# Kernel tuning notes

Hardware: AMD Instinct MI355X
Metric: run time of the kernel (lower is better)

Reference implementation:

```python
import jax, jax.numpy as jnp
from jax import lax
import numpy as np

B, T = 64, 512
IN, H, L, OUT = 128, 1024, 3, 1


def setup_inputs() -> dict:
    key = jax.random.key(0)
    ks = jax.random.split(key, 10)
    s = 1.0 / np.sqrt(H)  # PyTorch LSTM init: U(-1/sqrt(H), 1/sqrt(H))
    u = lambda k, shape: jax.random.uniform(k, shape, jnp.float32, -s, s)
    return {
        "x": jax.random.normal(ks[0], (B, T, IN), jnp.float32),
        "W_ih0": u(ks[1], (4 * H, IN)),
        "W_ih1": u(ks[2], (4 * H, H)),
        "W_ih2": u(ks[3], (4 * H, H)),
        "W_hh": u(ks[4], (L, 4 * H, H)),
        "b_ih": u(ks[5], (L, 4 * H)),
        "b_hh": u(ks[6], (L, 4 * H)),
        "fc_w": u(ks[7], (OUT, H)),
        "fc_b": u(ks[8], (OUT,)),
    }


def _lstm_layer(x, W_ih, W_hh_l, b_ih_l, b_hh_l):
    """One LSTM layer, batch_first input [B, T, F] -> [B, T, H].
    PyTorch gate order: i, f, g, o."""
    Bq = x.shape[0]
    Hh = W_hh_l.shape[1]
    # Precompute input projection for all timesteps (one big GEMM).
    xp = jnp.einsum("btf,gf->btg", x, W_ih) + b_ih_l + b_hh_l  # [B, T, 4H]
    xp = jnp.swapaxes(xp, 0, 1)  # [T, B, 4H] for scan

    def step(carry, gates_in):
        h, c = carry
        g = gates_in + h @ W_hh_l.T  # [B, 4H]
        i_, f_, g_, o_ = jnp.split(g, 4, axis=-1)
        c = jax.nn.sigmoid(f_) * c + jax.nn.sigmoid(i_) * jnp.tanh(g_)
        h = jax.nn.sigmoid(o_) * jnp.tanh(c)
        return (h, c), h

    h0 = jnp.zeros((Bq, Hh), x.dtype)
    _, hs = lax.scan(step, (h0, h0), xp)  # hs: [T, B, H]
    return jnp.swapaxes(hs, 0, 1)  # [B, T, H]


def reference(x, W_ih0, W_ih1, W_ih2, W_hh, b_ih, b_hh, fc_w, fc_b):
    # 3-layer LSTM (dropout disabled / eval mode for determinism).
    h = x
    for l, Wih in enumerate((W_ih0, W_ih1, W_ih2)):
        h = _lstm_layer(h, Wih, W_hh[l], b_ih[l], b_hh[l])
    # Original applies fc to all timesteps then takes [:, -1, :];
    # slicing first is mathematically identical and avoids a [B,T,OUT] buffer.
    return h[:, -1, :] @ fc_w.T + fc_b  # [B, OUT]
```

## Files before the change

kernel.cpp:

```cpp
#include <hip/hip_runtime.h>


#define TT 512
#define INF 128
#define HH 1024
#define NBLOCKS 192

typedef _Float16 f16x8 __attribute__((ext_vector_type(8)));
typedef float f32x4 __attribute__((ext_vector_type(4)));

#define HBUF_OFF 1024
#define XBUF_OFF (1024 + 786432)

__device__ __forceinline__ float sigmf(float x) { return 1.f / (1.f + __expf(-x)); }
__device__ __forceinline__ float tanhfast(float x) { return 1.f - 2.f / (__expf(2.f * x) + 1.f); }

__global__ void init_kernel(unsigned* ctrl, unsigned* hbuf_u32, float* out, const float* fcb) {
  int tid = blockIdx.x * 256 + threadIdx.x;
  if (tid < 196608) hbuf_u32[tid] = 0u;
  if (blockIdx.x == 0) {
    if (threadIdx.x < 2) ctrl[threadIdx.x] = 0u;
    if (threadIdx.x >= 64 && threadIdx.x < 128) out[threadIdx.x - 64] = fcb[0];
  }
}

__global__ void packx_kernel(const float* __restrict__ x, _Float16* __restrict__ xbuf) {
  int tid = blockIdx.x * 256 + threadIdx.x;
  int t = tid >> 10;
  int rem = tid & 1023;
  int kk = rem >> 8;
  int bt = (rem >> 6) & 3;
  int lane = rem & 63;
  int b = bt * 16 + (lane & 15);
  int k = kk * 32 + (lane >> 4) * 8;
  const float* src = x + ((size_t)b * TT + t) * INF + k;
  f16x8 v;
#pragma unroll
  for (int j = 0; j < 8; ++j) v[j] = (_Float16)src[j];
  ((f16x8*)xbuf)[tid] = v;
}

__device__ __forceinline__ f16x8 load_frag_agent(const unsigned long long* p) {
  union { unsigned long long u[2]; f16x8 v; } r;
  r.u[0] = __hip_atomic_load(p, __ATOMIC_RELAXED, __HIP_MEMORY_SCOPE_AGENT);
  r.u[1] = __hip_atomic_load(p + 1, __ATOMIC_RELAXED, __HIP_MEMORY_SCOPE_AGENT);
  return r.v;
}

__device__ __forceinline__ void loadB(f16x8 bf[4], int layer, int kk, int t, int rp,
                                      const f16x8* __restrict__ xb8,
                                      const unsigned long long* __restrict__ hb_u,
                                      int lane) {
  if (layer == 0 && kk < 4) {
    const f16x8* bsrc = xb8 + (size_t)t * 1024 + (size_t)kk * 256;
#pragma unroll
    for (int bt = 0; bt < 4; ++bt) bf[bt] = bsrc[bt * 64 + lane];
  } else {
    int buf, kidx;
    if (layer == 0) { buf = rp; kidx = kk - 4; }
    else if (layer == 1) {
      if (kk < 32) { buf = rp; kidx = kk; } else { buf = 2 + rp; kidx = kk - 32; }
    } else {
      if (kk < 32) { buf = 2 + rp; kidx = kk; } else { buf = 4 + rp; kidx = kk - 32; }
    }
#pragma unroll
    for (int bt = 0; bt < 4; ++bt)
      bf[bt] = load_frag_agent(hb_u + ((size_t)buf * 8192 + kidx * 256 + bt * 64 + lane) * 2);
  }
}

__global__ void __launch_bounds__(256, 1)
lstm_main(const float* __restrict__ Wih0, const float* __restrict__ Wih1,
          const float* __restrict__ Wih2, const float* __restrict__ Whh,
          const float* __restrict__ bih, const float* __restrict__ bhh,
          const float* __restrict__ fcw, float* __restrict__ out,
          unsigned* __restrict__ ctrl, _Float16* __restrict__ hbuf,
          const _Float16* __restrict__ xbuf) {
  const int blk = blockIdx.x;
  const int layer = blk >> 6;
  const int cu = blk & 63;
  const int tid = threadIdx.x;
  const int wave = tid >> 6;
  const int lane = tid & 63;
  const int m = lane & 15;
  const int q = lane >> 4;
  const int hid0 = cu << 4;

  const int KW = (layer == 0) ? 9 : 16;
  const int kk0 = wave * KW;

  __shared__ float part[4][4][16][66];
  __shared__ float fcacc[64];

  f16x8 fz;
#pragma unroll
  for (int j = 0; j < 8; ++j) fz[j] = (_Float16)0.f;

  f16x8 afrag[4][16];
#pragma unroll
  for (int g = 0; g < 4; ++g) {
#pragma unroll
    for (int kkl = 0; kkl < 16; ++kkl) {
      afrag[g][kkl] = fz;
      if (kkl < KW) {
        int kk = kk0 + kkl;
        int row = g * HH + hid0 + m;
        const float* src;
        if (layer == 0) {
          src = (kk < 4) ? (Wih0 + (size_t)row * INF + kk * 32)
                         : (Whh + (size_t)row * HH + (kk - 4) * 32);
        } else if (layer == 1) {
          src = (kk < 32) ? (Wih1 + (size_t)row * HH + kk * 32)
                          : (Whh + (size_t)(4 * HH) * HH + (size_t)row * HH + (kk - 32) * 32);
        } else {
          src = (kk < 32) ? (Wih2 + (size_t)row * HH + kk * 32)
                          : (Whh + (size_t)(8 * HH) * HH + (size_t)row * HH + (kk - 32) * 32);
        }
        src += q * 8;
        f16x8 v;
#pragma unroll
        for (int j = 0; j < 8; ++j) v[j] = (_Float16)src[j];
        afrag[g][kkl] = v;
      }
    }
  }

  const int bq = tid & 63;
  const int j4 = wave * 4;
  float biasv[4][4];
#pragma unroll
  for (int g = 0; g < 4; ++g)
#pragma unroll
    for (int i = 0; i < 4; ++i) {
      int row = layer * 4 * HH + g * HH + hid0 + j4 + i;
      biasv[g][i] = bih[row] + bhh[row];
    }
  float fcwv[4];
#pragma unroll
  for (int i = 0; i < 4; ++i) fcwv[i] = (layer == 2) ? fcw[hid0 + j4 + i] : 0.f;
  float cst[4] = {0.f, 0.f, 0.f, 0.f};

  const int jg = hid0 + j4;
  const int kkp = jg >> 5;
  const int qp = (jg >> 3) & 3;
  const int slot = (j4 & 7) >> 2;
  const int btp = bq >> 4;
  const int lanep = (bq & 15) + (qp << 4);

  const f16x8* xb8 = (const f16x8*)xbuf;
  const unsigned long long* hb_u = (const unsigned long long*)hbuf;
  unsigned long long* hb_w = (unsigned long long*)hbuf;

  const f32x4 zacc = {0.f, 0.f, 0.f, 0.f};

  for (int s = 0; s < TT + 2; ++s) {
    const int t = s - layer;
    const bool active = (t >= 0) && (t < TT);
    if (active) {
      const int rp = (s + 1) & 1;
      const int wp = s & 1;

      f32x4 acc[4][4];
#pragma unroll
      for (int g = 0; g < 4; ++g)
#pragma unroll
        for (int bt = 0; bt < 4; ++bt) acc[g][bt] = zacc;

      f16x8 bf0[4], bf1[4], bf2[4], bf3[4];
      loadB(bf0, layer, kk0 + 0, t, rp, xb8, hb_u, lane);
      loadB(bf1, layer, kk0 + 1, t, rp, xb8, hb_u, lane);
      loadB(bf2, layer, kk0 + 2, t, rp, xb8, hb_u, lane);
      loadB(bf3, layer, kk0 + 3, t, rp, xb8, hb_u, lane);

#define LSTM_STEP(KKL, BUF)                                                   \
      if ((KKL) < KW) {                                                       \
        _Pragma("unroll")                                                     \
        for (int g = 0; g < 4; ++g) {                                         \
          _Pragma("unroll")                                                   \
          for (int bt = 0; bt < 4; ++bt)                                      \
            acc[g][bt] = __builtin_amdgcn_mfma_f32_16x16x32_f16(              \
                afrag[g][(KKL)], BUF[bt], acc[g][bt], 0, 0, 0);               \
        }                                                                     \
        if ((KKL) + 4 < KW)                                                   \
          loadB(BUF, layer, kk0 + (KKL) + 4, t, rp, xb8, hb_u, lane);         \
      }

      LSTM_STEP(0, bf0)
      LSTM_STEP(1, bf1)
      LSTM_STEP(2, bf2)
      LSTM_STEP(3, bf3)
      LSTM_STEP(4, bf0)
      LSTM_STEP(5, bf1)
      LSTM_STEP(6, bf2)
      LSTM_STEP(7, bf3)
      LSTM_STEP(8, bf0)
      LSTM_STEP(9, bf1)
      LSTM_STEP(10, bf2)
      LSTM_STEP(11, bf3)
      LSTM_STEP(12, bf0)
      LSTM_STEP(13, bf1)
      LSTM_STEP(14, bf2)
      LSTM_STEP(15, bf3)
#undef LSTM_STEP

#pragma unroll
      for (int g = 0; g < 4; ++g)
#pragma unroll
        for (int bt = 0; bt < 4; ++bt)
#pragma unroll
          for (int r = 0; r < 4; ++r)
            part[wave][g][q * 4 + r][bt * 16 + m] = acc[g][bt][r];

      const bool do_fc = (layer == 2) && (t == TT - 1);
      if (do_fc && tid < 64) fcacc[tid] = 0.f;
      __syncthreads();

      float pre[4][4];
#pragma unroll
      for (int g = 0; g < 4; ++g)
#pragma unroll
        for (int i = 0; i < 4; ++i) pre[g][i] = biasv[g][i];
#pragma unroll
      for (int w = 0; w < 4; ++w)
#pragma unroll
        for (int g = 0; g < 4; ++g)
#pragma unroll
          for (int i = 0; i < 4; ++i) pre[g][i] += part[w][g][j4 + i][bq];

      union { unsigned long long u; _Float16 h4[4]; } pk;
      float facc = 0.f;
#pragma unroll
      for (int i = 0; i < 4; ++i) {
        float ig = sigmf(pre[0][i]);
        float fg = sigmf(pre[1][i]);
        float gg = tanhfast(pre[2][i]);
        float og = sigmf(pre[3][i]);
        cst[i] = fg * cst[i] + ig * gg;
        float hv = og * tanhfast(cst[i]);
        pk.h4[i] = (_Float16)hv;
        facc += hv * fcwv[i];
      }
      unsigned long long* pub =
          hb_w + ((size_t)(((layer * 2 + wp) * 32 + kkp) * 256 + btp * 64 + lanep)) * 2 + slot;
      __hip_atomic_store(pub, pk.u, __ATOMIC_RELAXED, __HIP_MEMORY_SCOPE_AGENT);

      if (do_fc) {
        atomicAdd(&fcacc[bq], facc);
        __syncthreads();
        if (tid < 64) atomicAdd(&out[tid], fcacc[tid]);
      }
    }

    __builtin_amdgcn_s_waitcnt(0);
    __syncthreads();
    if (tid == 0) {
      const unsigned target = (unsigned)(s + 1) * NBLOCKS;
      __hip_atomic_fetch_add(&ctrl[0], 1u, __ATOMIC_RELAXED, __HIP_MEMORY_SCOPE_AGENT);
      while (__hip_atomic_load(&ctrl[0], __ATOMIC_RELAXED, __HIP_MEMORY_SCOPE_AGENT) < target) {
        __builtin_amdgcn_s_sleep(2);
      }
    }
    __syncthreads();
  }
}

extern "C" void kernel_launch(void* const* d_in, const int* in_sizes, int n_in,
                              void* d_out, int out_size, void* d_ws, size_t ws_size,
                              hipStream_t stream) {
  const float* x    = (const float*)d_in[0];
  const float* Wih0 = (const float*)d_in[1];
  const float* Wih1 = (const float*)d_in[2];
  const float* Wih2 = (const float*)d_in[3];
  const float* Whh  = (const float*)d_in[4];
  const float* bih  = (const float*)d_in[5];
  const float* bhh  = (const float*)d_in[6];
  const float* fcw  = (const float*)d_in[7];
  const float* fcb  = (const float*)d_in[8];
  float* out = (float*)d_out;

  char* ws = (char*)d_ws;
  unsigned* ctrl = (unsigned*)ws;
  _Float16* hbuf = (_Float16*)(ws + HBUF_OFF);
  _Float16* xbuf = (_Float16*)(ws + XBUF_OFF);

  init_kernel<<<768, 256, 0, stream>>>(ctrl, (unsigned*)hbuf, out, fcb);
  packx_kernel<<<2048, 256, 0, stream>>>(x, xbuf);
  lstm_main<<<NBLOCKS, 256, 0, stream>>>(Wih0, Wih1, Wih2, Whh, bih, bhh, fcw,
                                         out, ctrl, hbuf, xbuf);
}
```

Baseline: 6.566 ms.

## Hand-pipeline B-fragment loads with inline asm dwordx4 and explicit vmcnt waits

Replaces the per-kk branching loadB (with paired 64-bit agent-scope atomic loads) with specialized per-layer k-loops that issue single 128-bit global loads using cache-bypass bits (sc0 sc1) for the h buffers and cached loads for x. Explicit s_waitcnt vmcnt counts and sched_barriers enforce a 4-deep software pipeline so the MFMAs for one k-slice overlap with loads for later slices. The aim is fewer memory instructions, no runtime layer/kk branching inside the loop, and tighter latency hiding. The risk is in coherence: the new loads are not atomics and rely on the sc bits to see other blocks' writes, and the hard-coded wait counts must stay correct.

```diff
diff --git a/kernel.cpp b/kernel.cpp
--- a/kernel.cpp
+++ b/kernel.cpp
@@ -40,33 +40,88 @@
   ((f16x8*)xbuf)[tid] = v;
 }
 
-__device__ __forceinline__ f16x8 load_frag_agent(const unsigned long long* p) {
-  union { unsigned long long u[2]; f16x8 v; } r;
-  r.u[0] = __hip_atomic_load(p, __ATOMIC_RELAXED, __HIP_MEMORY_SCOPE_AGENT);
-  r.u[1] = __hip_atomic_load(p + 1, __ATOMIC_RELAXED, __HIP_MEMORY_SCOPE_AGENT);
-  return r.v;
-}
-
-__device__ __forceinline__ void loadB(f16x8 bf[4], int layer, int kk, int t, int rp,
-                                      const f16x8* __restrict__ xb8,
-                                      const unsigned long long* __restrict__ hb_u,
-                                      int lane) {
-  if (layer == 0 && kk < 4) {
-    const f16x8* bsrc = xb8 + (size_t)t * 1024 + (size_t)kk * 256;
-#pragma unroll
-    for (int bt = 0; bt < 4; ++bt) bf[bt] = bsrc[bt * 64 + lane];
+__device__ __forceinline__ f16x8 load_ic16(const void* p) {
+  f16x8 v;
+  asm volatile("global_load_dwordx4 %0, %1, off sc0 sc1" : "=&v"(v) : "v"(p) : "memory");
+  return v;
+}
+__device__ __forceinline__ f16x8 load_ca16(const void* p) {
+  f16x8 v;
+  asm volatile("global_load_dwordx4 %0, %1, off" : "=&v"(v) : "v"(p) : "memory");
+  return v;
+}
+
+__device__ __forceinline__ void loadB4_ic(f16x8 bf[4], const char* base, int lane) {
+#pragma unroll
+  for (int bt = 0; bt < 4; ++bt) bf[bt] = load_ic16(base + (size_t)(bt * 64 + lane) * 16);
+}
+
+__device__ __forceinline__ void pfL0(f16x8 bf[4], int kk, const char* xb, const char* bLo,
+                                     int lane) {
+  if (kk < 4) {
+    const char* b = xb + (size_t)kk * 4096;
+#pragma unroll
+    for (int bt = 0; bt < 4; ++bt) bf[bt] = load_ca16(b + (size_t)(bt * 64 + lane) * 16);
   } else {
-    int buf, kidx;
-    if (layer == 0) { buf = rp; kidx = kk - 4; }
-    else if (layer == 1) {
-      if (kk < 32) { buf = rp; kidx = kk; } else { buf = 2 + rp; kidx = kk - 32; }
-    } else {
-      if (kk < 32) { buf = 2 + rp; kidx = kk; } else { buf = 4 + rp; kidx = kk - 32; }
-    }
-#pragma unroll
-    for (int bt = 0; bt < 4; ++bt)
-      bf[bt] = load_frag_agent(hb_u + ((size_t)buf * 8192 + kidx * 256 + bt * 64 + lane) * 2);
-  }
+    const char* b = bLo + (size_t)(kk - 4) * 4096;
+#pragma unroll
+    for (int bt = 0; bt < 4; ++bt) bf[bt] = load_ic16(b + (size_t)(bt * 64 + lane) * 16);
+  }
+}
+
+#define WAITV(N) asm volatile("s_waitcnt vmcnt(" #N ")" ::: "memory")
+#define SB0 __builtin_amdgcn_sched_barrier(0)
+#define MSTEP(KKL, BUF)                                                     \
+  {                                                                         \
+    _Pragma("unroll") for (int g = 0; g < 4; ++g) {                         \
+      _Pragma("unroll") for (int bt = 0; bt < 4; ++bt)                      \
+          acc[g][bt] = __builtin_amdgcn_mfma_f32_16x16x32_f16(              \
+              afrag[g][KKL], BUF[bt], acc[g][bt], 0, 0, 0);                 \
+    }                                                                       \
+  }
+
+__device__ __forceinline__ void kloop16(f32x4 acc[4][4], const f16x8 afrag[4][16], int kk0,
+                                        const char* bLo, const char* bHi, int lane) {
+  const char* wb = (kk0 < 32) ? bLo + (size_t)kk0 * 4096 : bHi + (size_t)(kk0 - 32) * 4096;
+  f16x8 b0[4], b1[4], b2[4], b3[4];
+  loadB4_ic(b0, wb + 0 * 4096, lane);
+  loadB4_ic(b1, wb + 1 * 4096, lane);
+  loadB4_ic(b2, wb + 2 * 4096, lane);
+  loadB4_ic(b3, wb + 3 * 4096, lane);
+  WAITV(12); SB0; MSTEP(0, b0);  loadB4_ic(b0, wb + 4 * 4096, lane);
+  WAITV(12); SB0; MSTEP(1, b1);  loadB4_ic(b1, wb + 5 * 4096, lane);
+  WAITV(12); SB0; MSTEP(2, b2);  loadB4_ic(b2, wb + 6 * 4096, lane);
+  WAITV(12); SB0; MSTEP(3, b3);  loadB4_ic(b3, wb + 7 * 4096, lane);
+  WAITV(12); SB0; MSTEP(4, b0);  loadB4_ic(b0, wb + 8 * 4096, lane);
+  WAITV(12); SB0; MSTEP(5, b1);  loadB4_ic(b1, wb + 9 * 4096, lane);
+  WAITV(12); SB0; MSTEP(6, b2);  loadB4_ic(b2, wb + 10 * 4096, lane);
+  WAITV(12); SB0; MSTEP(7, b3);  loadB4_ic(b3, wb + 11 * 4096, lane);
+  WAITV(12); SB0; MSTEP(8, b0);  loadB4_ic(b0, wb + 12 * 4096, lane);
+  WAITV(12); SB0; MSTEP(9, b1);  loadB4_ic(b1, wb + 13 * 4096, lane);
+  WAITV(12); SB0; MSTEP(10, b2); loadB4_ic(b2, wb + 14 * 4096, lane);
+  WAITV(12); SB0; MSTEP(11, b3); loadB4_ic(b3, wb + 15 * 4096, lane);
+  WAITV(12); SB0; MSTEP(12, b0);
+  WAITV(8);  SB0; MSTEP(13, b1);
+  WAITV(4);  SB0; MSTEP(14, b2);
+  WAITV(0);  SB0; MSTEP(15, b3);
+}
+
+__device__ __forceinline__ void kloop9(f32x4 acc[4][4], const f16x8 afrag[4][16], int kk0,
+                                       const char* xb, const char* bLo, int lane) {
+  f16x8 b0[4], b1[4], b2[4], b3[4];
+  pfL0(b0, kk0 + 0, xb, bLo, lane);
+  pfL0(b1, kk0 + 1, xb, bLo, lane);
+  pfL0(b2, kk0 + 2, xb, bLo, lane);
+  pfL0(b3, kk0 + 3, xb, bLo, lane);
+  WAITV(12); SB0; MSTEP(0, b0); pfL0(b0, kk0 + 4, xb, bLo, lane);
+  WAITV(12); SB0; MSTEP(1, b1); pfL0(b1, kk0 + 5, xb, bLo, lane);
+  WAITV(12); SB0; MSTEP(2, b2); pfL0(b2, kk0 + 6, xb, bLo, lane);
+  WAITV(12); SB0; MSTEP(3, b3); pfL0(b3, kk0 + 7, xb, bLo, lane);
+  WAITV(12); SB0; MSTEP(4, b0); pfL0(b0, kk0 + 8, xb, bLo, lane);
+  WAITV(12); SB0; MSTEP(5, b1);
+  WAITV(8);  SB0; MSTEP(6, b2);
+  WAITV(4);  SB0; MSTEP(7, b3);
+  WAITV(0);  SB0; MSTEP(8, b0);
 }
 
 __global__ void __launch_bounds__(256, 1)
@@ -147,8 +202,8 @@
   const int btp = bq >> 4;
   const int lanep = (bq & 15) + (qp << 4);
 
-  const f16x8* xb8 = (const f16x8*)xbuf;
-  const unsigned long long* hb_u = (const unsigned long long*)hbuf;
+  const char* const hb = (const char*)hbuf;
+  const char* const xbB = (const char*)xbuf;
   unsigned long long* hb_w = (unsigned long long*)hbuf;
 
   const f32x4 zacc = {0.f, 0.f, 0.f, 0.f};
@@ -166,42 +221,14 @@
 #pragma unroll
         for (int bt = 0; bt < 4; ++bt) acc[g][bt] = zacc;
 
-      f16x8 bf0[4], bf1[4], bf2[4], bf3[4];
-      loadB(bf0, layer, kk0 + 0, t, rp, xb8, hb_u, lane);
-      loadB(bf1, layer, kk0 + 1, t, rp, xb8, hb_u, lane);
-      loadB(bf2, layer, kk0 + 2, t, rp, xb8, hb_u, lane);
-      loadB(bf3, layer, kk0 + 3, t, rp, xb8, hb_u, lane);
-
-#define LSTM_STEP(KKL, BUF)                                                   \
-      if ((KKL) < KW) {                                                       \
-        _Pragma("unroll")                                                     \
-        for (int g = 0; g < 4; ++g) {                                         \
-          _Pragma("unroll")                                                   \
-          for (int bt = 0; bt < 4; ++bt)                                      \
-            acc[g][bt] = __builtin_amdgcn_mfma_f32_16x16x32_f16(              \
-                afrag[g][(KKL)], BUF[bt], acc[g][bt], 0, 0, 0);               \
-        }                                                                     \
-        if ((KKL) + 4 < KW)                                                   \
-          loadB(BUF, layer, kk0 + (KKL) + 4, t, rp, xb8, hb_u, lane);         \
-      }
-
-      LSTM_STEP(0, bf0)
-      LSTM_STEP(1, bf1)
-      LSTM_STEP(2, bf2)
-      LSTM_STEP(3, bf3)
-      LSTM_STEP(4, bf0)
-      LSTM_STEP(5, bf1)
-      LSTM_STEP(6, bf2)
-      LSTM_STEP(7, bf3)
-      LSTM_STEP(8, bf0)
-      LSTM_STEP(9, bf1)
-      LSTM_STEP(10, bf2)
-      LSTM_STEP(11, bf3)
-      LSTM_STEP(12, bf0)
-      LSTM_STEP(13, bf1)
-      LSTM_STEP(14, bf2)
-      LSTM_STEP(15, bf3)
-#undef LSTM_STEP
+      if (layer == 0) {
+        kloop9(acc, afrag, kk0, xbB + (size_t)t * 16384, hb + (size_t)rp * 131072, lane);
+      } else if (layer == 1) {
+        kloop16(acc, afrag, kk0, hb + (size_t)rp * 131072, hb + (size_t)(2 + rp) * 131072, lane);
+      } else {
+        kloop16(acc, afrag, kk0, hb + (size_t)(2 + rp) * 131072, hb + (size_t)(4 + rp) * 131072,
+                lane);
+      }
 
 #pragma unroll
       for (int g = 0; g < 4; ++g)
```

Result: faster. 5.323 ms (-18.9%).
